# Optimization experiments

Hardware: AMD Instinct MI355X
Metric: run time of the kernel (lower is better)

The kernel has to match this reference:

```python
import jax, jax.numpy as jnp
import numpy as np

N, IN_DIM, OUT_DIM = 8192, 1024, 1024

def setup_inputs() -> dict:
    key = jax.random.key(0)
    k1, k2, k3, k4 = jax.random.split(key, 4)
    return {
        "input_feature": jax.random.normal(k1, (N, IN_DIM), dtype=jnp.float32),
        "wq": jax.random.normal(k2, (IN_DIM, OUT_DIM), dtype=jnp.float32),
        "wk": jax.random.normal(k3, (IN_DIM, OUT_DIM), dtype=jnp.float32),
        "wv": jax.random.normal(k4, (IN_DIM, OUT_DIM), dtype=jnp.float32),
    }

def reference(input_feature, wq, wk, wv):
    # QKV projections: [N, out_dim]
    q = input_feature @ wq
    k = input_feature @ wk
    v = input_feature @ wv
    # Attention scores [N, N]; note: original applies NO 1/sqrt(d) scaling
    scores = q @ k.T
    attn = jax.nn.softmax(scores, axis=1)
    return attn @ v
```

## Files before the change

### kernel.cpp

```cpp
#include <hip/hip_runtime.h>
#include <hip/hip_bf16.h>
#include <math.h>

#define NROWS 8192
#define DIM   1024
#define CAP   256
#define MARGIN 120.0f

using f16x8 = __attribute__((ext_vector_type(8))) _Float16;
using f32x4 = __attribute__((ext_vector_type(4))) float;
typedef unsigned short u16;
typedef unsigned int   u32;

#define AS1 __attribute__((address_space(1)))
#define AS3 __attribute__((address_space(3)))

__global__ __launch_bounds__(256) void split2h(const float* __restrict__ X,
                                               u16* __restrict__ H,
                                               u16* __restrict__ L) {
    const int idx = (blockIdx.x * 256 + threadIdx.x) * 4;
    float4 x = *(const float4*)&X[idx];
    float c[4] = {x.x, x.y, x.z, x.w};
    u16 h[4], l[4];
#pragma unroll
    for (int i = 0; i < 4; ++i) {
        _Float16 hh = (_Float16)c[i];
        float r = c[i] - (float)hh;
        _Float16 ll = (_Float16)r;
        h[i] = *(u16*)&hh; l[i] = *(u16*)&ll;
    }
    *(ushort4*)&H[idx] = make_ushort4(h[0], h[1], h[2], h[3]);
    *(ushort4*)&L[idx] = make_ushort4(l[0], l[1], l[2], l[3]);
}

__global__ __launch_bounds__(256) void split_wvt(const float* __restrict__ W,
                                                 u16* __restrict__ H) {
    __shared__ float t[64][65];
    const int k0 = blockIdx.x * 64, n0 = blockIdx.y * 64;
    const int c = threadIdx.x & 63, r4 = threadIdx.x >> 6;
#pragma unroll
    for (int i = 0; i < 16; ++i) {
        int k = r4 + i * 4;
        t[k][c] = W[(size_t)(k0 + k) * DIM + n0 + c];
    }
    __syncthreads();
#pragma unroll
    for (int i = 0; i < 16; ++i) {
        int n = r4 + i * 4;
        _Float16 hb = (_Float16)t[c][n];
        H[(n0 + n) * DIM + k0 + c] = *(u16*)&hb;
    }
}

template<int NP>
__device__ __forceinline__ void gemm_lds(const u16* const (&Ap)[NP],
                                         const u16* const (&Bp)[NP],
                                         int row0, int col0, f32x4 (&acc)[4][4],
                                         short (&As)[2][2][4096], short (&Bs)[2][2][4096]) {
    const int tid = threadIdx.x;
    const int w = tid >> 6, lane = tid & 63;
    const int wy = w >> 1, wx = w & 1;
    const int quad = lane >> 4, r16 = lane & 15;

    const int    srow   = w * 32 + (lane >> 2);
    const int    schunk = (lane & 3) * 8;
    const size_t gA0 = (size_t)(row0 + srow) * DIM + schunk;
    const size_t gA1 = gA0 + (size_t)16 * DIM;
    const size_t gB0 = (size_t)(col0 + srow) * DIM + schunk;
    const size_t gB1 = gB0 + (size_t)16 * DIM;
    const int lds0 = (w * 32) * 32;
    const int lds1 = (w * 32 + 16) * 32;

    auto issue = [&](const u16* A, const u16* B, size_t k0, int buf) {
#pragma unroll
        for (int s = 0; s < 2; ++s) {
            const size_t ko = k0 + (size_t)s * 32;
            __builtin_amdgcn_global_load_lds((const AS1 u32*)(A + gA0 + ko), (AS3 u32*)&As[buf][s][lds0], 16, 0, 0);
            __builtin_amdgcn_global_load_lds((const AS1 u32*)(A + gA1 + ko), (AS3 u32*)&As[buf][s][lds1], 16, 0, 0);
            __builtin_amdgcn_global_load_lds((const AS1 u32*)(B + gB0 + ko), (AS3 u32*)&Bs[buf][s][lds0], 16, 0, 0);
            __builtin_amdgcn_global_load_lds((const AS1 u32*)(B + gB1 + ko), (AS3 u32*)&Bs[buf][s][lds1], 16, 0, 0);
        }
    };

    issue(Ap[0], Bp[0], 0, 0);

    int pp = 0;
#pragma unroll
    for (int p = 0; p < NP; ++p) {
        const u16* A = Ap[p];
        const u16* B = Bp[p];
        const u16* An = (p + 1 < NP) ? Ap[p + 1] : A;
        const u16* Bn = (p + 1 < NP) ? Bp[p + 1] : B;
        const bool more = (p + 1 < NP);
        for (int i = 0; i < 16; ++i) {
            __syncthreads();
            const int cur = pp, nxt = pp ^ 1;
            if (i < 15)      issue(A, B, (size_t)(i + 1) * 64, nxt);
            else if (more)   issue(An, Bn, 0, nxt);
#pragma unroll
            for (int s = 0; s < 2; ++s) {
                const short* AsC = As[cur][s];
                const short* BsC = Bs[cur][s];
                f16x8 af[4], bfr[4];
#pragma unroll
                for (int m = 0; m < 4; ++m)
                    af[m] = *(const f16x8*)&AsC[(wy * 64 + m * 16 + r16) * 32 + quad * 8];
#pragma unroll
                for (int n = 0; n < 4; ++n)
                    bfr[n] = *(const f16x8*)&BsC[(wx * 64 + n * 16 + r16) * 32 + quad * 8];
#pragma unroll
                for (int m = 0; m < 4; ++m)
#pragma unroll
                    for (int n = 0; n < 4; ++n)
                        acc[m][n] = __builtin_amdgcn_mfma_f32_16x16x32_f16(af[m], bfr[n], acc[m][n], 0, 0, 0);
            }
            pp ^= 1;
        }
    }
}

__global__ __launch_bounds__(256) void g_gemm(const u16* __restrict__ Wkh, const u16* __restrict__ Wkl,
                                              const u16* __restrict__ Wqh, const u16* __restrict__ Wql,
                                              float* __restrict__ Gt) {
    __shared__ short As[2][2][4096], Bs[2][2][4096];
    const int tid = threadIdx.x, w = tid >> 6, lane = tid & 63;
    const int wy = w >> 1, wx = w & 1, quad = lane >> 4, r16 = lane & 15;
    const int row0 = blockIdx.y * 128, col0 = blockIdx.x * 128;
    const u16* const Ap[3] = { Wkl, Wkh, Wkh };
    const u16* const Bp[3] = { Wqh, Wql, Wqh };
    f32x4 acc[4][4] = {};
    gemm_lds<3>(Ap, Bp, row0, col0, acc, As, Bs);
#pragma unroll
    for (int m = 0; m < 4; ++m)
#pragma unroll
        for (int n = 0; n < 4; ++n)
#pragma unroll
            for (int reg = 0; reg < 4; ++reg) {
                const int row = row0 + wy * 64 + m * 16 + quad * 4 + reg;
                const int col = col0 + wx * 64 + n * 16 + r16;
                Gt[row * DIM + col] = acc[m][n][reg];
            }
}

__global__ __launch_bounds__(256) void yv_gemm(const u16* __restrict__ Xh, const u16* __restrict__ Xl,
                                               const u16* __restrict__ Gth, const u16* __restrict__ Gtl,
                                               const u16* __restrict__ Wvth,
                                               float* __restrict__ Y, u16* __restrict__ Yh, u16* __restrict__ Vh) {
    __shared__ short As[2][2][4096], Bs[2][2][4096];
    const int tid = threadIdx.x, w = tid >> 6, lane = tid & 63;
    const int wy = w >> 1, wx = w & 1, quad = lane >> 4, r16 = lane & 15;
    const int id = blockIdx.x;
    const int z = id >> 9;
    const int within = id & 511;
    const int colt = within >> 6;
    const int rowt = within & 63;
    const int row0 = rowt * 128, col0 = colt * 128;
    f32x4 acc[4][4] = {};
    if (z == 0) {
        const u16* const Ap[3] = { Xl,  Xh,  Xh  };
        const u16* const Bp[3] = { Gth, Gtl, Gth };
        gemm_lds<3>(Ap, Bp, row0, col0, acc, As, Bs);
#pragma unroll
        for (int m = 0; m < 4; ++m)
#pragma unroll
            for (int n = 0; n < 4; ++n)
#pragma unroll
                for (int reg = 0; reg < 4; ++reg) {
                    const int row = row0 + wy * 64 + m * 16 + quad * 4 + reg;
                    const int col = col0 + wx * 64 + n * 16 + r16;
                    float v = acc[m][n][reg];
                    Y[row * DIM + col] = v;
                    _Float16 hb = (_Float16)v;
                    Yh[row * DIM + col] = *(u16*)&hb;
                }
    } else {
        const u16* const Ap[1] = { Xh };
        const u16* const Bp[1] = { Wvth };
        gemm_lds<1>(Ap, Bp, row0, col0, acc, As, Bs);
#pragma unroll
        for (int m = 0; m < 4; ++m)
#pragma unroll
            for (int n = 0; n < 4; ++n)
#pragma unroll
                for (int reg = 0; reg < 4; ++reg) {
                    const int row = row0 + wy * 64 + m * 16 + quad * 4 + reg;
                    const int col = col0 + wx * 64 + n * 16 + r16;
                    _Float16 hb = (_Float16)acc[m][n][reg];
                    Vh[row * DIM + col] = *(u16*)&hb;
                }
    }
}

__global__ __launch_bounds__(256) void filter_kernel(const u16* __restrict__ Yhp,
                                                     const u16* __restrict__ Xhp,
                                                     int* __restrict__ cnt,
                                                     int2* __restrict__ cand) {
    __shared__ short As[2][2][4096], Bs[2][2][4096];
    const int tid = threadIdx.x, w = tid >> 6, lane = tid & 63;
    const int wy = w >> 1, wx = w & 1, quad = lane >> 4, r16 = lane & 15;
    const int id = blockIdx.x;
    const int colt = id >> 6;
    const int rowt = id & 63;
    const int row0 = rowt * 128, col0 = colt * 128;

    const u16* const Ap[1] = { Yhp };
    const u16* const Bp[1] = { Xhp };
    f32x4 acc[4][4] = {};
    gemm_lds<1>(Ap, Bp, row0, col0, acc, As, Bs);

#pragma unroll
    for (int m = 0; m < 4; ++m) {
#pragma unroll
        for (int reg = 0; reg < 4; ++reg) {
            float mx = fmaxf(fmaxf(acc[m][0][reg], acc[m][1][reg]),
                             fmaxf(acc[m][2][reg], acc[m][3][reg]));
            mx = fmaxf(mx, __shfl_xor(mx, 1, 64));
            mx = fmaxf(mx, __shfl_xor(mx, 2, 64));
            mx = fmaxf(mx, __shfl_xor(mx, 4, 64));
            mx = fmaxf(mx, __shfl_xor(mx, 8, 64));
            const float th = mx - MARGIN;
            const int row = row0 + wy * 64 + m * 16 + quad * 4 + reg;
#pragma unroll
            for (int n = 0; n < 4; ++n) {
                float s = acc[m][n][reg];
                if (s >= th) {
                    int pos = atomicAdd(&cnt[row], 1);
                    if (pos < CAP)
                        cand[(size_t)row * CAP + pos] =
                            make_int2(col0 + wx * 64 + n * 16 + r16, __float_as_int(s));
                }
            }
        }
    }
}

__global__ __launch_bounds__(256) void finalize_kernel(const float* __restrict__ Y,
                                                       const float* __restrict__ X,
                                                       const u16* __restrict__ Vh,
                                                       const int* __restrict__ cnt,
                                                       const int2* __restrict__ cand,
                                                       float* __restrict__ out) {
    const int i = blockIdx.x;
    const int tid = threadIdx.x;
    const int w = tid >> 6, lane = tid & 63;
    __shared__ float  red[256];
    __shared__ int    surv[64];
    __shared__ double sprec[64];
    __shared__ float  wgt[64];
    __shared__ int    nsurv;

    const int c = min(cnt[i], CAP);
    float m = -3.0e38f;
    for (int t = tid; t < c; t += 256)
        m = fmaxf(m, __int_as_float(cand[(size_t)i * CAP + t].y));
    red[tid] = m;
    __syncthreads();
    for (int s = 128; s > 0; s >>= 1) {
        if (tid < s) red[tid] = fmaxf(red[tid], red[tid + s]);
        __syncthreads();
    }
    const float th = red[0] - MARGIN;
    if (tid == 0) nsurv = 0;
    __syncthreads();
    for (int t = tid; t < c; t += 256) {
        int2 e = cand[(size_t)i * CAP + t];
        if (__int_as_float(e.y) >= th) {
            int p = atomicAdd(&nsurv, 1);
            if (p < 64) surv[p] = e.x;
        }
    }
    __syncthreads();
    const int ns = min(nsurv, 64);
    for (int u = w; u < ns; u += 4) {
        const int j = surv[u];
        double a = 0.0;
        for (int d = lane; d < DIM; d += 64)
            a += (double)Y[(size_t)i * DIM + d] * (double)X[(size_t)j * DIM + d];
#pragma unroll
        for (int o = 32; o > 0; o >>= 1)
            a += __shfl_down(a, o, 64);
        if (lane == 0) sprec[u] = a;
    }
    __syncthreads();
    if (tid == 0) {
        double mm = -1.0e300;
        for (int u = 0; u < ns; ++u) mm = fmax(mm, sprec[u]);
        double l = 0.0;
        for (int u = 0; u < ns; ++u) l += exp(sprec[u] - mm);
        for (int u = 0; u < ns; ++u) wgt[u] = (float)(exp(sprec[u] - mm) / l);
    }
    __syncthreads();
    for (int d = tid; d < DIM; d += 256) {
        float o = 0.f;
        for (int u = 0; u < ns; ++u) {
            _Float16 hv = *(const _Float16*)&Vh[(size_t)surv[u] * DIM + d];
            o += wgt[u] * (float)hv;
        }
        out[(size_t)i * DIM + d] = o;
    }
}

extern "C" void kernel_launch(void* const* d_in, const int* in_sizes, int n_in,
                              void* d_out, int out_size, void* d_ws, size_t ws_size,
                              hipStream_t stream) {
    const float* X  = (const float*)d_in[0];
    const float* wq = (const float*)d_in[1];
    const float* wk = (const float*)d_in[2];
    const float* wv = (const float*)d_in[3];
    float* out = (float*)d_out;

    char* ws = (char*)d_ws;
    const size_t MB = 1024 * 1024;
    u16*   Xh   = (u16*)(ws +   0 * MB);
    u16*   Xl   = (u16*)(ws +  16 * MB);
    u16*   Wqh  = (u16*)(ws +  32 * MB);
    u16*   Wql  = (u16*)(ws +  34 * MB);
    u16*   Wkh  = (u16*)(ws +  36 * MB);
    u16*   Wkl  = (u16*)(ws +  38 * MB);
    u16*   Wvth = (u16*)(ws +  40 * MB);
    float* Gt   = (float*)(ws + 42 * MB);
    u16*   Gth  = (u16*)(ws +  46 * MB);
    u16*   Gtl  = (u16*)(ws +  48 * MB);
    float* Y    = (float*)(ws + 64 * MB);
    u16*   Yh   = (u16*)(ws +  96 * MB);
    u16*   Vh   = (u16*)(ws + 112 * MB);
    int*   cnt  = (int*)(ws + 128 * MB);
    int2*  cand = (int2*)(ws + 129 * MB);

    hipMemsetAsync(cnt, 0, (size_t)NROWS * 4, stream);

    split2h<<<NROWS * DIM / 1024, 256, 0, stream>>>(X, Xh, Xl);
    split2h<<<DIM * DIM / 1024, 256, 0, stream>>>(wq, Wqh, Wql);
    split2h<<<DIM * DIM / 1024, 256, 0, stream>>>(wk, Wkh, Wkl);
    split_wvt<<<dim3(16, 16), 256, 0, stream>>>(wv, Wvth);

    g_gemm<<<dim3(8, 8), 256, 0, stream>>>(Wkh, Wkl, Wqh, Wql, Gt);
    split2h<<<DIM * DIM / 1024, 256, 0, stream>>>(Gt, Gth, Gtl);

    yv_gemm<<<1024, 256, 0, stream>>>(Xh, Xl, Gth, Gtl, Wvth, Y, Yh, Vh);

    filter_kernel<<<4096, 256, 0, stream>>>(Yh, Xh, cnt, cand);

    finalize_kernel<<<NROWS, 256, 0, stream>>>(Y, X, Vh, cnt, cand, out);
}
```

Measured before the change: 639.3 us.

## Use per-wave private LDS buffers with swizzle to drop block barriers in GEMMs

Replaces the block-shared LDS tiles with per-wavefront private double buffers. Each wave loads its own 64-row A and B slices directly into LDS, waits with s_waitcnt vmcnt instead of __syncthreads, and uses an XOR swizzle to reduce LDS bank conflicts. The goal is to remove block-wide barrier stalls and bank conflicts. In exchange, data shared between waves is no longer reused: each wave refetches its A and B rows, which doubles global and L2 traffic, and the K step per iteration shrinks to 32.

```diff
diff --git a/kernel.cpp b/kernel.cpp
--- a/kernel.cpp
+++ b/kernel.cpp
@@ -53,33 +53,31 @@
 }
 
 template<int NP>
-__device__ __forceinline__ void gemm_lds(const u16* const (&Ap)[NP],
-                                         const u16* const (&Bp)[NP],
-                                         int row0, int col0, f32x4 (&acc)[4][4],
-                                         short (&As)[2][2][4096], short (&Bs)[2][2][4096]) {
-    const int tid = threadIdx.x;
-    const int w = tid >> 6, lane = tid & 63;
+__device__ __forceinline__ void gemm_wp(const u16* const (&Ap)[NP],
+                                        const u16* const (&Bp)[NP],
+                                        int row0, int col0,
+                                        f32x4 (&acc)[4][4],
+                                        short (&Ls)[2][4096]) {
+    const int tid  = threadIdx.x;
+    const int lane = tid & 63;
+    const int w    = tid >> 6;
     const int wy = w >> 1, wx = w & 1;
     const int quad = lane >> 4, r16 = lane & 15;
 
-    const int    srow   = w * 32 + (lane >> 2);
-    const int    schunk = (lane & 3) * 8;
-    const size_t gA0 = (size_t)(row0 + srow) * DIM + schunk;
-    const size_t gA1 = gA0 + (size_t)16 * DIM;
-    const size_t gB0 = (size_t)(col0 + srow) * DIM + schunk;
-    const size_t gB1 = gB0 + (size_t)16 * DIM;
-    const int lds0 = (w * 32) * 32;
-    const int lds1 = (w * 32 + 16) * 32;
-
-    auto issue = [&](const u16* A, const u16* B, size_t k0, int buf) {
-#pragma unroll
-        for (int s = 0; s < 2; ++s) {
-            const size_t ko = k0 + (size_t)s * 32;
-            __builtin_amdgcn_global_load_lds((const AS1 u32*)(A + gA0 + ko), (AS3 u32*)&As[buf][s][lds0], 16, 0, 0);
-            __builtin_amdgcn_global_load_lds((const AS1 u32*)(A + gA1 + ko), (AS3 u32*)&As[buf][s][lds1], 16, 0, 0);
-            __builtin_amdgcn_global_load_lds((const AS1 u32*)(B + gB0 + ko), (AS3 u32*)&Bs[buf][s][lds0], 16, 0, 0);
-            __builtin_amdgcn_global_load_lds((const AS1 u32*)(B + gB1 + ko), (AS3 u32*)&Bs[buf][s][lds1], 16, 0, 0);
-        }
+    const int    srow   = lane >> 2;
+    const int    schunk = ((lane & 3) ^ ((lane >> 3) & 3)) * 8;
+    const size_t gA = (size_t)(row0 + wy * 64 + srow) * DIM + schunk;
+    const size_t gB = (size_t)(col0 + wx * 64 + srow) * DIM + schunk;
+
+    auto issue = [&](const u16* A, const u16* B, size_t ko, int buf) {
+#pragma unroll
+        for (int t = 0; t < 4; ++t)
+            __builtin_amdgcn_global_load_lds((const AS1 u32*)(A + gA + (size_t)t * 16 * DIM + ko),
+                                             (AS3 u32*)&Ls[buf][t * 512], 16, 0, 0);
+#pragma unroll
+        for (int t = 0; t < 4; ++t)
+            __builtin_amdgcn_global_load_lds((const AS1 u32*)(B + gB + (size_t)t * 16 * DIM + ko),
+                                             (AS3 u32*)&Ls[buf][2048 + t * 512], 16, 0, 0);
     };
 
     issue(Ap[0], Bp[0], 0, 0);
@@ -87,33 +85,35 @@
     int pp = 0;
 #pragma unroll
     for (int p = 0; p < NP; ++p) {
-        const u16* A = Ap[p];
-        const u16* B = Bp[p];
+        const u16* A  = Ap[p];
+        const u16* B  = Bp[p];
         const u16* An = (p + 1 < NP) ? Ap[p + 1] : A;
         const u16* Bn = (p + 1 < NP) ? Bp[p + 1] : B;
         const bool more = (p + 1 < NP);
-        for (int i = 0; i < 16; ++i) {
-            __syncthreads();
+        for (int i = 0; i < 32; ++i) {
             const int cur = pp, nxt = pp ^ 1;
-            if (i < 15)      issue(A, B, (size_t)(i + 1) * 64, nxt);
-            else if (more)   issue(An, Bn, 0, nxt);
-#pragma unroll
-            for (int s = 0; s < 2; ++s) {
-                const short* AsC = As[cur][s];
-                const short* BsC = Bs[cur][s];
-                f16x8 af[4], bfr[4];
-#pragma unroll
-                for (int m = 0; m < 4; ++m)
-                    af[m] = *(const f16x8*)&AsC[(wy * 64 + m * 16 + r16) * 32 + quad * 8];
+            if (i < 31) {
+                issue(A, B, (size_t)(i + 1) * 32, nxt);
+                asm volatile("s_waitcnt vmcnt(8)" ::: "memory");
+            } else if (more) {
+                issue(An, Bn, 0, nxt);
+                asm volatile("s_waitcnt vmcnt(8)" ::: "memory");
+            } else {
+                asm volatile("s_waitcnt vmcnt(0)" ::: "memory");
+            }
+            const int swz = (quad ^ ((r16 >> 1) & 3)) * 8;
+            f16x8 af[4], bfr[4];
+#pragma unroll
+            for (int m = 0; m < 4; ++m)
+                af[m] = *(const f16x8*)&Ls[cur][(m * 16 + r16) * 32 + swz];
+#pragma unroll
+            for (int n = 0; n < 4; ++n)
+                bfr[n] = *(const f16x8*)&Ls[cur][2048 + (n * 16 + r16) * 32 + swz];
+#pragma unroll
+            for (int m = 0; m < 4; ++m)
 #pragma unroll
                 for (int n = 0; n < 4; ++n)
-                    bfr[n] = *(const f16x8*)&BsC[(wx * 64 + n * 16 + r16) * 32 + quad * 8];
-#pragma unroll
-                for (int m = 0; m < 4; ++m)
-#pragma unroll
-                    for (int n = 0; n < 4; ++n)
-                        acc[m][n] = __builtin_amdgcn_mfma_f32_16x16x32_f16(af[m], bfr[n], acc[m][n], 0, 0, 0);
-            }
+                    acc[m][n] = __builtin_amdgcn_mfma_f32_16x16x32_f16(af[m], bfr[n], acc[m][n], 0, 0, 0);
             pp ^= 1;
         }
     }
@@ -122,14 +122,14 @@
 __global__ __launch_bounds__(256) void g_gemm(const u16* __restrict__ Wkh, const u16* __restrict__ Wkl,
                                               const u16* __restrict__ Wqh, const u16* __restrict__ Wql,
                                               float* __restrict__ Gt) {
-    __shared__ short As[2][2][4096], Bs[2][2][4096];
+    __shared__ short Ls[4][2][4096];
     const int tid = threadIdx.x, w = tid >> 6, lane = tid & 63;
     const int wy = w >> 1, wx = w & 1, quad = lane >> 4, r16 = lane & 15;
     const int row0 = blockIdx.y * 128, col0 = blockIdx.x * 128;
     const u16* const Ap[3] = { Wkl, Wkh, Wkh };
     const u16* const Bp[3] = { Wqh, Wql, Wqh };
     f32x4 acc[4][4] = {};
-    gemm_lds<3>(Ap, Bp, row0, col0, acc, As, Bs);
+    gemm_wp<3>(Ap, Bp, row0, col0, acc, Ls[w]);
 #pragma unroll
     for (int m = 0; m < 4; ++m)
 #pragma unroll
@@ -146,7 +146,7 @@
                                                const u16* __restrict__ Gth, const u16* __restrict__ Gtl,
                                                const u16* __restrict__ Wvth,
                                                float* __restrict__ Y, u16* __restrict__ Yh, u16* __restrict__ Vh) {
-    __shared__ short As[2][2][4096], Bs[2][2][4096];
+    __shared__ short Ls[4][2][4096];
     const int tid = threadIdx.x, w = tid >> 6, lane = tid & 63;
     const int wy = w >> 1, wx = w & 1, quad = lane >> 4, r16 = lane & 15;
     const int id = blockIdx.x;
@@ -159,7 +159,7 @@
     if (z == 0) {
         const u16* const Ap[3] = { Xl,  Xh,  Xh  };
         const u16* const Bp[3] = { Gth, Gtl, Gth };
-        gemm_lds<3>(Ap, Bp, row0, col0, acc, As, Bs);
+        gemm_wp<3>(Ap, Bp, row0, col0, acc, Ls[w]);
 #pragma unroll
         for (int m = 0; m < 4; ++m)
 #pragma unroll
@@ -176,7 +176,7 @@
     } else {
         const u16* const Ap[1] = { Xh };
         const u16* const Bp[1] = { Wvth };
-        gemm_lds<1>(Ap, Bp, row0, col0, acc, As, Bs);
+        gemm_wp<1>(Ap, Bp, row0, col0, acc, Ls[w]);
 #pragma unroll
         for (int m = 0; m < 4; ++m)
 #pragma unroll
@@ -195,7 +195,7 @@
                                                      const u16* __restrict__ Xhp,
                                                      int* __restrict__ cnt,
                                                      int2* __restrict__ cand) {
-    __shared__ short As[2][2][4096], Bs[2][2][4096];
+    __shared__ short Ls[4][2][4096];
     const int tid = threadIdx.x, w = tid >> 6, lane = tid & 63;
     const int wy = w >> 1, wx = w & 1, quad = lane >> 4, r16 = lane & 15;
     const int id = blockIdx.x;
@@ -206,7 +206,7 @@
     const u16* const Ap[1] = { Yhp };
     const u16* const Bp[1] = { Xhp };
     f32x4 acc[4][4] = {};
-    gemm_lds<1>(Ap, Bp, row0, col0, acc, As, Bs);
+    gemm_wp<1>(Ap, Bp, row0, col0, acc, Ls[w]);
 
 #pragma unroll
     for (int m = 0; m < 4; ++m) {
```

Result: no change. 651.7 us (+1.9%).
